# Performance work log

Measured on AMD Instinct MI355X. Metric: run time of the kernel, lower is better.

The kernel has to match this reference:

```python
import jax, jax.numpy as jnp
import numpy as np

N_NODES = 50000
N_EDGES = 800000
D = 64
L = 5
NUM_GRAPHS = 512
NOUT = 768

def setup_inputs() -> dict:
    key = jax.random.key(0)
    ks = jax.random.split(key, 8)
    s = 1.0 / np.sqrt(D)
    x = jax.random.normal(ks[0], (N_NODES, D), dtype=jnp.float32)
    edge_index = jax.random.randint(ks[1], (2, N_EDGES), 0, N_NODES, dtype=jnp.int64)
    batch = jnp.sort(jax.random.randint(ks[2], (N_NODES,), 0, NUM_GRAPHS, dtype=jnp.int64))
    return {
        'x': x,
        'edge_index': edge_index,
        'batch': batch,
        'gin_w1': jax.random.normal(ks[3], (L, D, D), dtype=jnp.float32) * s,
        'gin_b1': jnp.zeros((L, D), dtype=jnp.float32),
        'gin_w2': jax.random.normal(ks[4], (L, D, D), dtype=jnp.float32) * s,
        'gin_b2': jnp.zeros((L, D), dtype=jnp.float32),
        'eps': jnp.zeros((L,), dtype=jnp.float32),
        'w_h1': jax.random.normal(ks[5], (D, D), dtype=jnp.float32) * s,
        'b_h1': jnp.zeros((D,), dtype=jnp.float32),
        'w_h2': jax.random.normal(ks[6], (D, NOUT), dtype=jnp.float32) * s,
        'b_h2': jnp.zeros((NOUT,), dtype=jnp.float32),
    }

def reference(x, edge_index, batch, gin_w1, gin_b1, gin_w2, gin_b2, eps, w_h1, b_h1, w_h2, b_h2):
    src, dst = edge_index[0], edge_index[1]
    n = x.shape[0]
    h = x
    for l in range(L):
        # GINConv: mlp((1+eps)*x_i + sum_{j->i} x_j)  (scatter-add over edges)
        agg = jax.ops.segment_sum(h[src], dst, num_segments=n)
        z = (1.0 + eps[l]) * h + agg
        z = jax.nn.relu(z @ gin_w1[l] + gin_b1[l]) @ gin_w2[l] + gin_b2[l]
        h = jax.nn.relu(z) if l < L - 1 else z  # activation between conv layers only
    # global mean pool over graphs
    sums = jax.ops.segment_sum(h, batch, num_segments=NUM_GRAPHS)
    cnts = jax.ops.segment_sum(jnp.ones((n, 1), h.dtype), batch, num_segments=NUM_GRAPHS)
    pooled = sums / jnp.maximum(cnts, 1.0)
    # MLP head
    return jax.nn.relu(pooled @ w_h1 + b_h1) @ w_h2 + b_h2
```

## Files before the change

### kernel.cpp

```cpp
#include <hip/hip_runtime.h>
#include <hip/hip_fp16.h>

#define N_NODES 50000
#define N_EDGES 800000
#define D 64
#define NLAYER 5
#define NUM_GRAPHS 512
#define NOUT 768
#define ZSCALE 0.0625f
#define WSCALE 16.0f

#define SUPW 512
#define NSUPER 98
#define PART_EDGES 4096
#define PART_BLOCKS 196
#define CSR_CAP 16384

typedef _Float16 f16x8 __attribute__((ext_vector_type(8)));
typedef float f32x4 __attribute__((ext_vector_type(4)));


__global__ __launch_bounds__(128) void zero_super_kernel(int* __restrict__ superCnt) {
    int i = threadIdx.x;
    if (i < NSUPER) superCnt[i] = 0;
}

__global__ __launch_bounds__(256) void hist_super_kernel(const int* __restrict__ dst,
                                                         int* __restrict__ superCnt) {
    __shared__ int h[NSUPER];
    int t = threadIdx.x;
    if (t < NSUPER) h[t] = 0;
    __syncthreads();
    int e0 = blockIdx.x * PART_EDGES;
    int eN = min(e0 + PART_EDGES, N_EDGES) - e0;
    for (int i = t; i < eN; i += 256) atomicAdd(&h[dst[e0 + i] >> 9], 1);
    __syncthreads();
    if (t < NSUPER) atomicAdd(&superCnt[t], h[t]);
}

__global__ __launch_bounds__(128) void scan_super_kernel(const int* __restrict__ superCnt,
                                                         int* __restrict__ superBase,
                                                         int* __restrict__ superCur) {
    if (threadIdx.x == 0) {
        int run = 0;
        for (int s = 0; s < NSUPER; ++s) {
            superBase[s] = run; superCur[s] = run; run += superCnt[s];
        }
        superBase[NSUPER] = run;
    }
}

__global__ __launch_bounds__(1024) void partition_kernel(
    const int* __restrict__ src, const int* __restrict__ dst,
    int* __restrict__ superCur, unsigned* __restrict__ ebuf) {
    __shared__ int hist[NSUPER];
    __shared__ int pref[NSUPER + 1];
    __shared__ int base[NSUPER];
    __shared__ int curs[NSUPER];
    __shared__ unsigned out[PART_EDGES];
    int t = threadIdx.x;
    int e0 = blockIdx.x * PART_EDGES;
    int eN = min(e0 + PART_EDGES, N_EDGES) - e0;
    if (t < NSUPER) hist[t] = 0;
    __syncthreads();
    for (int i = t; i < eN; i += 1024) atomicAdd(&hist[dst[e0 + i] >> 9], 1);
    __syncthreads();
    if (t == 0) {
        int run = 0;
        for (int s = 0; s < NSUPER; ++s) { pref[s] = run; run += hist[s]; }
        pref[NSUPER] = run;
    }
    __syncthreads();
    if (t < NSUPER) {
        base[t] = atomicAdd(&superCur[t], hist[t]);
        curs[t] = pref[t];
    }
    __syncthreads();
    for (int i = t; i < eN; i += 1024) {
        int d = dst[e0 + i];
        int s = d >> 9;
        int p = atomicAdd(&curs[s], 1);
        out[p] = ((unsigned)(d & 511) << 16) | (unsigned)src[e0 + i];
    }
    __syncthreads();
    for (int i = t; i < eN; i += 1024) {
        int lo = 0, hi = NSUPER;
        while (lo + 1 < hi) { int mid = (lo + hi) >> 1; if (pref[mid] <= i) lo = mid; else hi = mid; }
        ebuf[base[lo] + (i - pref[lo])] = out[i];
    }
}

__global__ __launch_bounds__(512) void buildcsr_kernel(const unsigned* __restrict__ ebuf,
                                                       const int* __restrict__ superBase,
                                                       unsigned short* __restrict__ csr16,
                                                       int* __restrict__ row_ptr) {
    __shared__ int hist[SUPW];
    __shared__ int pref[SUPW];
    __shared__ int cur[SUPW];
    __shared__ unsigned short out16[CSR_CAP];
    int s = blockIdx.x, t = threadIdx.x;
    int beg = superBase[s], end = superBase[s + 1];
    int cnt = end - beg;
    hist[t] = 0;
    __syncthreads();
    for (int i = beg + t; i < end; i += 512)
        atomicAdd(&hist[(ebuf[i] >> 16) & 511], 1);
    __syncthreads();
    pref[t] = hist[t];
    __syncthreads();
    #pragma unroll
    for (int off = 1; off < 512; off <<= 1) {
        int u = (t >= off) ? pref[t - off] : 0;
        __syncthreads();
        pref[t] += u;
        __syncthreads();
    }
    int excl = pref[t] - hist[t];
    int node = s * SUPW + t;
    if (node < N_NODES) row_ptr[node] = beg + excl;
    if (s == NSUPER - 1 && t == 0) row_ptr[N_NODES] = N_EDGES;
    cur[t] = excl;
    __syncthreads();
    for (int i = beg + t; i < end; i += 512) {
        unsigned u = ebuf[i];
        int p = atomicAdd(&cur[(u >> 16) & 511], 1);
        unsigned short sv = (unsigned short)(u & 0xffff);
        if (p < CSR_CAP) out16[p] = sv;
        else csr16[beg + p] = sv;
    }
    __syncthreads();
    int lim = min(cnt, CSR_CAP);
    for (int i = t; i < lim; i += 512) csr16[beg + i] = out16[i];
}

__global__ __launch_bounds__(256) void tohalf_kernel(const float* __restrict__ in,
                                                     __half2* __restrict__ out) {
    int i = blockIdx.x * 256 + threadIdx.x;
    if (i < N_NODES * D / 2) {
        float2 v = ((const float2*)in)[i];
        out[i] = __floats2half2_rn(v.x, v.y);
    }
}

template <bool LAST>
__global__ __launch_bounds__(256, 4) void gin_fused_kernel(
    const __half2* __restrict__ h2in, __half2* __restrict__ h16out,
    float* __restrict__ hout_f32,
    const int* __restrict__ row_ptr, const unsigned short* __restrict__ csr16,
    const float* __restrict__ eps, int l,
    const float* __restrict__ w1, const float* __restrict__ b1,
    const float* __restrict__ w2, const float* __restrict__ b2) {
    __shared__ __align__(16) __half Z[D][72];
    __shared__ __align__(16) __half Wt[D][72];
    __shared__ float B1s[D], B2s[D];

    int t = threadIdx.x;
    int row0 = blockIdx.x * D;

    int nl = t >> 2;
    int q  = t & 3;
    int node = row0 + nl;
    bool nvalid = node < N_NODES;
    int beg = nvalid ? row_ptr[node] : 0;
    int end = nvalid ? row_ptr[node + 1] : 0;

    {
        const float4* ws = (const float4*)w1;
        #pragma unroll
        for (int i = 0; i < 4; ++i) {
            int g = t + i * 256;
            float4 v = ws[g];
            int k = g >> 4, n0 = (g & 15) << 2;
            Wt[n0 + 0][k] = __float2half_rn(v.x * WSCALE);
            Wt[n0 + 1][k] = __float2half_rn(v.y * WSCALE);
            Wt[n0 + 2][k] = __float2half_rn(v.z * WSCALE);
            Wt[n0 + 3][k] = __float2half_rn(v.w * WSCALE);
        }
        if (t < D) { B1s[t] = b1[t]; B2s[t] = b2[t]; }
    }

    float epsl = 1.0f + eps[l];
    const f16x8* hrows = (const f16x8*)h2in;

    float acc[16];
    {
        f16x8 u0 = {}, u1 = {};
        if (nvalid) {
            u0 = hrows[(size_t)node * 8 + 2 * q];
            u1 = hrows[(size_t)node * 8 + 2 * q + 1];
        }
        #pragma unroll
        for (int j = 0; j < 8; ++j) {
            acc[j]     = (float)u0[j] * epsl;
            acc[8 + j] = (float)u1[j] * epsl;
        }
    }
    for (int i = beg; i < end; i += 4) {
        #pragma unroll
        for (int k = 0; k < 4; ++k) {
            bool valid = (i + k < end);
            int ii = valid ? (i + k) : beg;
            float mult = valid ? 1.0f : 0.0f;
            int sidx = csr16[ii];
            f16x8 u0 = hrows[(size_t)sidx * 8 + 2 * q];
            f16x8 u1 = hrows[(size_t)sidx * 8 + 2 * q + 1];
            #pragma unroll
            for (int j = 0; j < 8; ++j) {
                acc[j]     = fmaf((float)u0[j], mult, acc[j]);
                acc[8 + j] = fmaf((float)u1[j], mult, acc[8 + j]);
            }
        }
    }
    {
        f16x8 z0, z1;
        #pragma unroll
        for (int j = 0; j < 8; ++j) {
            z0[j] = (_Float16)(acc[j] * ZSCALE);
            z1[j] = (_Float16)(acc[8 + j] * ZSCALE);
        }
        *(f16x8*)&Z[nl][q * 16]     = z0;
        *(f16x8*)&Z[nl][q * 16 + 8] = z1;
    }
    __syncthreads();

    int m  = t & 15;
    int hi = (t >> 4) & 3;
    int w  = t >> 6;

    float4 w2r[4];
    {
        const float4* ws = (const float4*)w2;
        #pragma unroll
        for (int i = 0; i < 4; ++i) w2r[i] = ws[t + i * 256];
    }

    f16x8 a0 = *(const f16x8*)&Z[w * 16 + m][hi * 8];
    f16x8 a1 = *(const f16x8*)&Z[w * 16 + m][32 + hi * 8];
    f32x4 c1[4];
    #pragma unroll
    for (int n = 0; n < 4; ++n) {
        f16x8 bf0 = *(const f16x8*)&Wt[n * 16 + m][hi * 8];
        f16x8 bf1 = *(const f16x8*)&Wt[n * 16 + m][32 + hi * 8];
        f32x4 c = {0.f, 0.f, 0.f, 0.f};
        c = __builtin_amdgcn_mfma_f32_16x16x32_f16(a0, bf0, c, 0, 0, 0);
        c = __builtin_amdgcn_mfma_f32_16x16x32_f16(a1, bf1, c, 0, 0, 0);
        c1[n] = c;
    }
    __syncthreads();

    #pragma unroll
    for (int n = 0; n < 4; ++n) {
        int col = n * 16 + m;
        #pragma unroll
        for (int r = 0; r < 4; ++r) {
            int row = w * 16 + hi * 4 + r;
            float v = c1[n][r] + B1s[col];
            Z[row][col] = __float2half_rn(fmaxf(v, 0.f) * ZSCALE);
        }
    }
    {
        #pragma unroll
        for (int i = 0; i < 4; ++i) {
            int g = t + i * 256;
            float4 v = w2r[i];
            int k = g >> 4, n0 = (g & 15) << 2;
            Wt[n0 + 0][k] = __float2half_rn(v.x * WSCALE);
            Wt[n0 + 1][k] = __float2half_rn(v.y * WSCALE);
            Wt[n0 + 2][k] = __float2half_rn(v.z * WSCALE);
            Wt[n0 + 3][k] = __float2half_rn(v.w * WSCALE);
        }
    }
    __syncthreads();

    f16x8 y0 = *(const f16x8*)&Z[w * 16 + m][hi * 8];
    f16x8 y1 = *(const f16x8*)&Z[w * 16 + m][32 + hi * 8];
    f32x4 c2[4];
    #pragma unroll
    for (int n = 0; n < 4; ++n) {
        f16x8 bf0 = *(const f16x8*)&Wt[n * 16 + m][hi * 8];
        f16x8 bf1 = *(const f16x8*)&Wt[n * 16 + m][32 + hi * 8];
        f32x4 c = {0.f, 0.f, 0.f, 0.f};
        c = __builtin_amdgcn_mfma_f32_16x16x32_f16(y0, bf0, c, 0, 0, 0);
        c = __builtin_amdgcn_mfma_f32_16x16x32_f16(y1, bf1, c, 0, 0, 0);
        c2[n] = c;
    }
    #pragma unroll
    for (int n = 0; n < 4; ++n) {
        int col = n * 16 + m;
        #pragma unroll
        for (int r = 0; r < 4; ++r) {
            int grow = row0 + w * 16 + hi * 4 + r;
            if (grow < N_NODES) {
                float o = c2[n][r] + B2s[col];
                if (LAST) {
                    hout_f32[(size_t)grow * D + col] = o;
                } else {
                    ((__half*)h16out)[(size_t)grow * D + col] = __float2half_rn(fmaxf(o, 0.f));
                }
            }
        }
    }
}

template <bool RELU>
__global__ __launch_bounds__(256) void gemm64_kernel(const float* __restrict__ X,
                                                     const float* __restrict__ Wg,
                                                     const float* __restrict__ bg,
                                                     float* __restrict__ Y, int nrows) {
    __shared__ float At[D][D + 1];
    __shared__ float Ws[D][D];
    __shared__ float Bs[D];

    int t = threadIdx.x;
    int row0 = blockIdx.x * D;
    {
        const float4* wsrc = (const float4*)Wg;
        float4* wdst = (float4*)Ws;
        #pragma unroll
        for (int i = 0; i < 4; ++i) wdst[t + i * 256] = wsrc[t + i * 256];
        if (t < D) Bs[t] = bg[t];
    }
    #pragma unroll
    for (int ii = 0; ii < 4; ++ii) {
        int i = t + ii * 256;
        int r = i >> 4;
        int c4 = i & 15;
        int row = row0 + r;
        float4 v = (row < nrows) ? ((const float4*)(X + (size_t)row * D))[c4]
                                 : make_float4(0.f, 0.f, 0.f, 0.f);
        At[c4 * 4 + 0][r] = v.x;
        At[c4 * 4 + 1][r] = v.y;
        At[c4 * 4 + 2][r] = v.z;
        At[c4 * 4 + 3][r] = v.w;
    }
    __syncthreads();

    int tx = t & 15, ty = t >> 4;
    int i0 = ty * 4, j0 = tx * 4;
    float acc[4][4];
    #pragma unroll
    for (int a = 0; a < 4; ++a)
        #pragma unroll
        for (int c = 0; c < 4; ++c) acc[a][c] = Bs[j0 + c];
    for (int k = 0; k < D; ++k) {
        float4 av = *(const float4*)&At[k][i0];
        float4 wv = *(const float4*)&Ws[k][j0];
        acc[0][0] += av.x * wv.x; acc[0][1] += av.x * wv.y; acc[0][2] += av.x * wv.z; acc[0][3] += av.x * wv.w;
        acc[1][0] += av.y * wv.x; acc[1][1] += av.y * wv.y; acc[1][2] += av.y * wv.z; acc[1][3] += av.y * wv.w;
        acc[2][0] += av.z * wv.x; acc[2][1] += av.z * wv.y; acc[2][2] += av.z * wv.z; acc[2][3] += av.z * wv.w;
        acc[3][0] += av.w * wv.x; acc[3][1] += av.w * wv.y; acc[3][2] += av.w * wv.z; acc[3][3] += av.w * wv.w;
    }
    #pragma unroll
    for (int a = 0; a < 4; ++a) {
        int row = row0 + i0 + a;
        if (row < nrows) {
            float4 v = make_float4(acc[a][0], acc[a][1], acc[a][2], acc[a][3]);
            if (RELU) {
                v.x = fmaxf(v.x, 0.f); v.y = fmaxf(v.y, 0.f);
                v.z = fmaxf(v.z, 0.f); v.w = fmaxf(v.w, 0.f);
            }
            ((float4*)(Y + (size_t)row * D))[tx] = v;
        }
    }
}

__device__ __forceinline__ int lower_bound_i(const int* a, int n, int key) {
    int lo = 0, hi = n;
    while (lo < hi) {
        int mid = (lo + hi) >> 1;
        if (a[mid] < key) lo = mid + 1;
        else hi = mid;
    }
    return lo;
}

__global__ __launch_bounds__(256) void pool_mean_kernel(const float* __restrict__ h,
                                                        const int* __restrict__ batch,
                                                        float* __restrict__ pooled) {
    __shared__ float red[4][D];
    int g = blockIdx.x;
    int t = threadIdx.x;
    int w = t >> 6, d = t & 63;
    int start = lower_bound_i(batch, N_NODES, g);
    int end = lower_bound_i(batch, N_NODES, g + 1);
    float sum = 0.f;
    for (int i = start + w; i < end; i += 4) sum += h[(size_t)i * D + d];
    red[w][d] = sum;
    __syncthreads();
    if (w == 0) {
        int cnt = end - start;
        float tot = red[0][d] + red[1][d] + red[2][d] + red[3][d];
        pooled[g * D + d] = tot / (float)(cnt > 0 ? cnt : 1);
    }
}

__global__ __launch_bounds__(256) void head2_kernel(const float* __restrict__ tin,
                                                    const float* __restrict__ w,
                                                    const float* __restrict__ b,
                                                    float* __restrict__ out) {
    __shared__ float trow[D];
    int i = blockIdx.y;
    int j = blockIdx.x * 256 + threadIdx.x;
    if (threadIdx.x < D) trow[threadIdx.x] = tin[i * D + threadIdx.x];
    __syncthreads();
    float acc = b[j];
    #pragma unroll
    for (int k = 0; k < D; ++k) acc += trow[k] * w[k * NOUT + j];
    out[(size_t)i * NOUT + j] = acc;
}

extern "C" void kernel_launch(void* const* d_in, const int* in_sizes, int n_in,
                              void* d_out, int out_size, void* d_ws, size_t ws_size,
                              hipStream_t stream) {
    const float* x   = (const float*)d_in[0];
    const int*   ei  = (const int*)d_in[1];
    const int*   src = ei;
    const int*   dst = ei + N_EDGES;
    const int* batch = (const int*)d_in[2];
    const float* gw1 = (const float*)d_in[3];
    const float* gb1 = (const float*)d_in[4];
    const float* gw2 = (const float*)d_in[5];
    const float* gb2 = (const float*)d_in[6];
    const float* eps = (const float*)d_in[7];
    const float* wh1 = (const float*)d_in[8];
    const float* bh1 = (const float*)d_in[9];
    const float* wh2 = (const float*)d_in[10];
    const float* bh2 = (const float*)d_in[11];
    float* out = (float*)d_out;

    char* p = (char*)d_ws;
    float* hfin   = (float*)p; p += (size_t)N_NODES * D * 4;
    float* pooled = (float*)p; p += (size_t)NUM_GRAPHS * D * 4;
    float* thead  = (float*)p; p += (size_t)NUM_GRAPHS * D * 4;
    __half2* h16a = (__half2*)p; p += (size_t)N_NODES * D * 2;
    __half2* h16b = (__half2*)p; p += (size_t)N_NODES * D * 2;
    unsigned* ebuf = (unsigned*)p; p += (size_t)N_EDGES * 4;
    int* superCnt  = (int*)p; p += 128 * 4;
    int* superBase = (int*)p; p += 128 * 4;
    int* superCur  = (int*)p; p += 128 * 4;
    int* row_ptr   = (int*)p; p += 50052 * 4;
    unsigned short* csr16 = (unsigned short*)p; p += (size_t)N_EDGES * 2;

    const int nodeBlocks = (N_NODES + D - 1) / D;

    zero_super_kernel<<<1, 128, 0, stream>>>(superCnt);
    hist_super_kernel<<<PART_BLOCKS, 256, 0, stream>>>(dst, superCnt);
    scan_super_kernel<<<1, 128, 0, stream>>>(superCnt, superBase, superCur);
    partition_kernel<<<PART_BLOCKS, 1024, 0, stream>>>(src, dst, superCur, ebuf);
    buildcsr_kernel<<<NSUPER, 512, 0, stream>>>(ebuf, superBase, csr16, row_ptr);

    tohalf_kernel<<<(N_NODES * D / 2 + 255) / 256, 256, 0, stream>>>(x, h16a);

    const __half2* hin = h16a;
    __half2* hout = h16b;
    for (int l = 0; l < NLAYER; ++l) {
        if (l < NLAYER - 1)
            gin_fused_kernel<false><<<nodeBlocks, 256, 0, stream>>>(
                hin, hout, hfin, row_ptr, csr16, eps, l,
                gw1 + (size_t)l * D * D, gb1 + (size_t)l * D,
                gw2 + (size_t)l * D * D, gb2 + (size_t)l * D);
        else
            gin_fused_kernel<true><<<nodeBlocks, 256, 0, stream>>>(
                hin, hout, hfin, row_ptr, csr16, eps, l,
                gw1 + (size_t)l * D * D, gb1 + (size_t)l * D,
                gw2 + (size_t)l * D * D, gb2 + (size_t)l * D);
        const __half2* tmp = hin;
        hin = hout;
        hout = (__half2*)tmp;
    }

    pool_mean_kernel<<<NUM_GRAPHS, 256, 0, stream>>>(hfin, batch, pooled);
    gemm64_kernel<true><<<(NUM_GRAPHS + D - 1) / D, 256, 0, stream>>>(pooled, wh1, bh1, thead, NUM_GRAPHS);
    head2_kernel<<<dim3(NOUT / 256, NUM_GRAPHS), 256, 0, stream>>>(thead, wh2, bh2, out);
}
```

Before: 167.9 us.

## Fuse tail kernels, shrink GIN tile, and streamline CSR build

The fp16 conversion of x moves into the histogram kernel, and each packed edge now carries its superbin so the binary search disappears. The block scan is replaced with wave shuffles. The GIN layer uses 32-node tiles with 8 threads per node and batches 8 gathered rows per iteration for more memory parallelism and occupancy. Pooling and both head GEMMs are fused into one 32-block kernel, which cuts launches but makes the tail much less parallel.

Result: slower. 330.6 us (+96.9%).

```diff
diff --git a/kernel.cpp b/kernel.cpp
--- a/kernel.cpp
+++ b/kernel.cpp
@@ -16,6 +16,9 @@
 #define PART_BLOCKS 196
 #define CSR_CAP 16384
 
+#define GIN_TILE 32
+#define GIN_BLOCKS 1563
+
 typedef _Float16 f16x8 __attribute__((ext_vector_type(8)));
 typedef float f32x4 __attribute__((ext_vector_type(4)));
 
@@ -26,11 +29,21 @@
 }
 
 __global__ __launch_bounds__(256) void hist_super_kernel(const int* __restrict__ dst,
-                                                         int* __restrict__ superCnt) {
+                                                         int* __restrict__ superCnt,
+                                                         const float* __restrict__ xin,
+                                                         __half2* __restrict__ xh) {
     __shared__ int h[NSUPER];
     int t = threadIdx.x;
     if (t < NSUPER) h[t] = 0;
     __syncthreads();
+    {
+        int gid = blockIdx.x * 256 + t;
+        int tot = N_NODES * D / 2;
+        for (int i = gid; i < tot; i += PART_BLOCKS * 256) {
+            float2 v = ((const float2*)xin)[i];
+            xh[i] = __floats2half2_rn(v.x, v.y);
+        }
+    }
     int e0 = blockIdx.x * PART_EDGES;
     int eN = min(e0 + PART_EDGES, N_EDGES) - e0;
     for (int i = t; i < eN; i += 256) atomicAdd(&h[dst[e0 + i] >> 9], 1);
@@ -80,13 +93,13 @@
         int d = dst[e0 + i];
         int s = d >> 9;
         int p = atomicAdd(&curs[s], 1);
-        out[p] = ((unsigned)(d & 511) << 16) | (unsigned)src[e0 + i];
+        out[p] = ((unsigned)s << 25) | ((unsigned)(d & 511) << 16) | (unsigned)src[e0 + i];
     }
     __syncthreads();
     for (int i = t; i < eN; i += 1024) {
-        int lo = 0, hi = NSUPER;
-        while (lo + 1 < hi) { int mid = (lo + hi) >> 1; if (pref[mid] <= i) lo = mid; else hi = mid; }
-        ebuf[base[lo] + (i - pref[lo])] = out[i];
+        unsigned u = out[i];
+        int s = u >> 25;
+        ebuf[base[s] + (i - pref[s])] = u;
     }
 }
 
@@ -95,10 +108,12 @@
                                                        unsigned short* __restrict__ csr16,
                                                        int* __restrict__ row_ptr) {
     __shared__ int hist[SUPW];
-    __shared__ int pref[SUPW];
     __shared__ int cur[SUPW];
+    __shared__ int waveSum[8];
+    __shared__ int waveOff[8];
     __shared__ unsigned short out16[CSR_CAP];
     int s = blockIdx.x, t = threadIdx.x;
+    int lane = t & 63, wv = t >> 6;
     int beg = superBase[s], end = superBase[s + 1];
     int cnt = end - beg;
     hist[t] = 0;
@@ -106,16 +121,22 @@
     for (int i = beg + t; i < end; i += 512)
         atomicAdd(&hist[(ebuf[i] >> 16) & 511], 1);
     __syncthreads();
-    pref[t] = hist[t];
-    __syncthreads();
+    int own = hist[t];
+    int x = own;
     #pragma unroll
-    for (int off = 1; off < 512; off <<= 1) {
-        int u = (t >= off) ? pref[t - off] : 0;
-        __syncthreads();
-        pref[t] += u;
-        __syncthreads();
-    }
-    int excl = pref[t] - hist[t];
+    for (int off = 1; off < 64; off <<= 1) {
+        int y = __shfl_up(x, off, 64);
+        if (lane >= off) x += y;
+    }
+    if (lane == 63) waveSum[wv] = x;
+    __syncthreads();
+    if (t == 0) {
+        int run = 0;
+        #pragma unroll
+        for (int w = 0; w < 8; ++w) { waveOff[w] = run; run += waveSum[w]; }
+    }
+    __syncthreads();
+    int excl = x + waveOff[wv] - own;
     int node = s * SUPW + t;
     if (node < N_NODES) row_ptr[node] = beg + excl;
     if (s == NSUPER - 1 && t == 0) row_ptr[N_NODES] = N_EDGES;
@@ -133,32 +154,23 @@
     for (int i = t; i < lim; i += 512) csr16[beg + i] = out16[i];
 }
 
-__global__ __launch_bounds__(256) void tohalf_kernel(const float* __restrict__ in,
-                                                     __half2* __restrict__ out) {
-    int i = blockIdx.x * 256 + threadIdx.x;
-    if (i < N_NODES * D / 2) {
-        float2 v = ((const float2*)in)[i];
-        out[i] = __floats2half2_rn(v.x, v.y);
-    }
-}
-
 template <bool LAST>
-__global__ __launch_bounds__(256, 4) void gin_fused_kernel(
+__global__ __launch_bounds__(256, 6) void gin_fused_kernel(
     const __half2* __restrict__ h2in, __half2* __restrict__ h16out,
     float* __restrict__ hout_f32,
     const int* __restrict__ row_ptr, const unsigned short* __restrict__ csr16,
     const float* __restrict__ eps, int l,
     const float* __restrict__ w1, const float* __restrict__ b1,
     const float* __restrict__ w2, const float* __restrict__ b2) {
-    __shared__ __align__(16) __half Z[D][72];
+    __shared__ __align__(16) __half Z[GIN_TILE][72];
     __shared__ __align__(16) __half Wt[D][72];
     __shared__ float B1s[D], B2s[D];
 
     int t = threadIdx.x;
-    int row0 = blockIdx.x * D;
-
-    int nl = t >> 2;
-    int q  = t & 3;
+    int row0 = blockIdx.x * GIN_TILE;
+
+    int nl = t >> 3;
+    int o  = t & 7;
     int node = row0 + nl;
     bool nvalid = node < N_NODES;
     int beg = nvalid ? row_ptr[node] : 0;
@@ -182,50 +194,45 @@
     float epsl = 1.0f + eps[l];
     const f16x8* hrows = (const f16x8*)h2in;
 
-    float acc[16];
-    {
-        f16x8 u0 = {}, u1 = {};
-        if (nvalid) {
-            u0 = hrows[(size_t)node * 8 + 2 * q];
-            u1 = hrows[(size_t)node * 8 + 2 * q + 1];
-        }
-        #pragma unroll
-        for (int j = 0; j < 8; ++j) {
-            acc[j]     = (float)u0[j] * epsl;
-            acc[8 + j] = (float)u1[j] * epsl;
-        }
-    }
-    for (int i = beg; i < end; i += 4) {
-        #pragma unroll
-        for (int k = 0; k < 4; ++k) {
+    float acc[8];
+    {
+        f16x8 u = {};
+        if (nvalid) u = hrows[(size_t)node * 8 + o];
+        #pragma unroll
+        for (int j = 0; j < 8; ++j) acc[j] = (float)u[j] * epsl;
+    }
+    for (int i = beg; i < end; i += 8) {
+        int sidx[8]; float mult[8];
+        #pragma unroll
+        for (int k = 0; k < 8; ++k) {
             bool valid = (i + k < end);
             int ii = valid ? (i + k) : beg;
-            float mult = valid ? 1.0f : 0.0f;
-            int sidx = csr16[ii];
-            f16x8 u0 = hrows[(size_t)sidx * 8 + 2 * q];
-            f16x8 u1 = hrows[(size_t)sidx * 8 + 2 * q + 1];
+            mult[k] = valid ? 1.0f : 0.0f;
+            sidx[k] = csr16[ii];
+        }
+        f16x8 u[8];
+        #pragma unroll
+        for (int k = 0; k < 8; ++k) u[k] = hrows[(size_t)sidx[k] * 8 + o];
+        #pragma unroll
+        for (int k = 0; k < 8; ++k)
             #pragma unroll
-            for (int j = 0; j < 8; ++j) {
-                acc[j]     = fmaf((float)u0[j], mult, acc[j]);
-                acc[8 + j] = fmaf((float)u1[j], mult, acc[8 + j]);
-            }
-        }
-    }
-    {
-        f16x8 z0, z1;
-        #pragma unroll
-        for (int j = 0; j < 8; ++j) {
-            z0[j] = (_Float16)(acc[j] * ZSCALE);
-            z1[j] = (_Float16)(acc[8 + j] * ZSCALE);
-        }
-        *(f16x8*)&Z[nl][q * 16]     = z0;
-        *(f16x8*)&Z[nl][q * 16 + 8] = z1;
-    }
-    __syncthreads();
-
-    int m  = t & 15;
-    int hi = (t >> 4) & 3;
-    int w  = t >> 6;
+            for (int j = 0; j < 8; ++j)
+                acc[j] = fmaf((float)u[k][j], mult[k], acc[j]);
+    }
+    {
+        f16x8 z;
+        #pragma unroll
+        for (int j = 0; j < 8; ++j) z[j] = (_Float16)(acc[j] * ZSCALE);
+        *(f16x8*)&Z[nl][o * 8] = z;
+    }
+    __syncthreads();
+
+    int lane = t & 63;
+    int v  = t >> 6;
+    int m  = lane & 15;
+    int hi = lane >> 4;
+    int mt = v & 1;
+    int np = v >> 1;
 
     float4 w2r[4];
     {
@@ -234,132 +241,72 @@
         for (int i = 0; i < 4; ++i) w2r[i] = ws[t + i * 256];
     }
 
-    f16x8 a0 = *(const f16x8*)&Z[w * 16 + m][hi * 8];
-    f16x8 a1 = *(const f16x8*)&Z[w * 16 + m][32 + hi * 8];
-    f32x4 c1[4];
+    f16x8 a0 = *(const f16x8*)&Z[mt * 16 + m][hi * 8];
+    f16x8 a1 = *(const f16x8*)&Z[mt * 16 + m][32 + hi * 8];
+    f32x4 c1[2];
     #pragma unroll
-    for (int n = 0; n < 4; ++n) {
+    for (int nn = 0; nn < 2; ++nn) {
+        int n = np * 2 + nn;
         f16x8 bf0 = *(const f16x8*)&Wt[n * 16 + m][hi * 8];
         f16x8 bf1 = *(const f16x8*)&Wt[n * 16 + m][32 + hi * 8];
         f32x4 c = {0.f, 0.f, 0.f, 0.f};
         c = __builtin_amdgcn_mfma_f32_16x16x32_f16(a0, bf0, c, 0, 0, 0);
         c = __builtin_amdgcn_mfma_f32_16x16x32_f16(a1, bf1, c, 0, 0, 0);
-        c1[n] = c;
+        c1[nn] = c;
     }
     __syncthreads();
 
     #pragma unroll
-    for (int n = 0; n < 4; ++n) {
-        int col = n * 16 + m;
+    for (int nn = 0; nn < 2; ++nn) {
+        int col = (np * 2 + nn) * 16 + m;
         #pragma unroll
         for (int r = 0; r < 4; ++r) {
-            int row = w * 16 + hi * 4 + r;
-            float v = c1[n][r] + B1s[col];
-            Z[row][col] = __float2half_rn(fmaxf(v, 0.f) * ZSCALE);
+            int row = mt * 16 + hi * 4 + r;
+            float val = c1[nn][r] + B1s[col];
+            Z[row][col] = __float2half_rn(fmaxf(val, 0.f) * ZSCALE);
         }
     }
     {
         #pragma unroll
         for (int i = 0; i < 4; ++i) {
             int g = t + i * 256;
-            float4 v = w2r[i];
+            float4 vv = w2r[i];
             int k = g >> 4, n0 = (g & 15) << 2;
-            Wt[n0 + 0][k] = __float2half_rn(v.x * WSCALE);
-            Wt[n0 + 1][k] = __float2half_rn(v.y * WSCALE);
-            Wt[n0 + 2][k] = __float2half_rn(v.z * WSCALE);
-            Wt[n0 + 3][k] = __float2half_rn(v.w * WSCALE);
-        }
-    }
-    __syncthreads();
-
-    f16x8 y0 = *(const f16x8*)&Z[w * 16 + m][hi * 8];
-    f16x8 y1 = *(const f16x8*)&Z[w * 16 + m][32 + hi * 8];
-    f32x4 c2[4];
+            Wt[n0 + 0][k] = __float2half_rn(vv.x * WSCALE);
+            Wt[n0 + 1][k] = __float2half_rn(vv.y * WSCALE);
+            Wt[n0 + 2][k] = __float2half_rn(vv.z * WSCALE);
+            Wt[n0 + 3][k] = __float2half_rn(vv.w * WSCALE);
+        }
+    }
+    __syncthreads();
+
+    f16x8 y0 = *(const f16x8*)&Z[mt * 16 + m][hi * 8];
+    f16x8 y1 = *(const f16x8*)&Z[mt * 16 + m][32 + hi * 8];
+    f32x4 c2[2];
     #pragma unroll
-    for (int n = 0; n < 4; ++n) {
+    for (int nn = 0; nn < 2; ++nn) {
+        int n = np * 2 + nn;
         f16x8 bf0 = *(const f16x8*)&Wt[n * 16 + m][hi * 8];
         f16x8 bf1 = *(const f16x8*)&Wt[n * 16 + m][32 + hi * 8];
         f32x4 c = {0.f, 0.f, 0.f, 0.f};
         c = __builtin_amdgcn_mfma_f32_16x16x32_f16(y0, bf0, c, 0, 0, 0);
         c = __builtin_amdgcn_mfma_f32_16x16x32_f16(y1, bf1, c, 0, 0, 0);
-        c2[n] = c;
+        c2[nn] = c;
     }
     #pragma unroll
-    for (int n = 0; n < 4; ++n) {
-        int col = n * 16 + m;
+    for (int nn = 0; nn < 2; ++nn) {
+        int col = (np * 2 + nn) * 16 + m;
         #pragma unroll
         for (int r = 0; r < 4; ++r) {
-            int grow = row0 + w * 16 + hi * 4 + r;
+            int grow = row0 + mt * 16 + hi * 4 + r;
             if (grow < N_NODES) {
-                float o = c2[n][r] + B2s[col];
+                float ov = c2[nn][r] + B2s[col];
                 if (LAST) {
-                    hout_f32[(size_t)grow * D + col] = o;
+                    hout_f32[(size_t)grow * D + col] = ov;
                 } else {
-                    ((__half*)h16out)[(size_t)grow * D + col] = __float2half_rn(fmaxf(o, 0.f));
+                    ((__half*)h16out)[(size_t)grow * D + col] = __float2half_rn(fmaxf(ov, 0.f));
                 }
             }
-        }
-    }
-}
-
-template <bool RELU>
-__global__ __launch_bounds__(256) void gemm64_kernel(const float* __restrict__ X,
-                                                     const float* __restrict__ Wg,
-                                                     const float* __restrict__ bg,
-                                                     float* __restrict__ Y, int nrows) {
-    __shared__ float At[D][D + 1];
-    __shared__ float Ws[D][D];
-    __shared__ float Bs[D];
-
-    int t = threadIdx.x;
-    int row0 = blockIdx.x * D;
-    {
-        const float4* wsrc = (const float4*)Wg;
-        float4* wdst = (float4*)Ws;
-        #pragma unroll
-        for (int i = 0; i < 4; ++i) wdst[t + i * 256] = wsrc[t + i * 256];
-        if (t < D) Bs[t] = bg[t];
-    }
-    #pragma unroll
-    for (int ii = 0; ii < 4; ++ii) {
-        int i = t + ii * 256;
-        int r = i >> 4;
-        int c4 = i & 15;
-        int row = row0 + r;
-        float4 v = (row < nrows) ? ((const float4*)(X + (size_t)row * D))[c4]
-                                 : make_float4(0.f, 0.f, 0.f, 0.f);
-        At[c4 * 4 + 0][r] = v.x;
-        At[c4 * 4 + 1][r] = v.y;
-        At[c4 * 4 + 2][r] = v.z;
-        At[c4 * 4 + 3][r] = v.w;
-    }
-    __syncthreads();
-
-    int tx = t & 15, ty = t >> 4;
-    int i0 = ty * 4, j0 = tx * 4;
-    float acc[4][4];
-    #pragma unroll
-    for (int a = 0; a < 4; ++a)
-        #pragma unroll
-        for (int c = 0; c < 4; ++c) acc[a][c] = Bs[j0 + c];
-    for (int k = 0; k < D; ++k) {
-        float4 av = *(const float4*)&At[k][i0];
-        float4 wv = *(const float4*)&Ws[k][j0];
-        acc[0][0] += av.x * wv.x; acc[0][1] += av.x * wv.y; acc[0][2] += av.x * wv.z; acc[0][3] += av.x * wv.w;
-        acc[1][0] += av.y * wv.x; acc[1][1] += av.y * wv.y; acc[1][2] += av.y * wv.z; acc[1][3] += av.y * wv.w;
-        acc[2][0] += av.z * wv.x; acc[2][1] += av.z * wv.y; acc[2][2] += av.z * wv.z; acc[2][3] += av.z * wv.w;
-        acc[3][0] += av.w * wv.x; acc[3][1] += av.w * wv.y; acc[3][2] += av.w * wv.z; acc[3][3] += av.w * wv.w;
-    }
-    #pragma unroll
-    for (int a = 0; a < 4; ++a) {
-        int row = row0 + i0 + a;
-        if (row < nrows) {
-            float4 v = make_float4(acc[a][0], acc[a][1], acc[a][2], acc[a][3]);
-            if (RELU) {
-                v.x = fmaxf(v.x, 0.f); v.y = fmaxf(v.y, 0.f);
-                v.z = fmaxf(v.z, 0.f); v.w = fmaxf(v.w, 0.f);
-            }
-            ((float4*)(Y + (size_t)row * D))[tx] = v;
         }
     }
 }
@@ -374,39 +321,69 @@
     return lo;
 }
 
-__global__ __launch_bounds__(256) void pool_mean_kernel(const float* __restrict__ h,
-                                                        const int* __restrict__ batch,
-                                                        float* __restrict__ pooled) {
-    __shared__ float red[4][D];
-    int g = blockIdx.x;
+#define TAIL_G 16
+__global__ __launch_bounds__(256) void pool_head_kernel(
+    const float* __restrict__ hfin, const int* __restrict__ batch,
+    const float* __restrict__ wh1, const float* __restrict__ bh1,
+    const float* __restrict__ wh2, const float* __restrict__ bh2,
+    float* __restrict__ out) {
+    __shared__ float P[TAIL_G][D + 1];
+    __shared__ float Wh[D * D];
+    __shared__ float T[TAIL_G][D + 1];
+
     int t = threadIdx.x;
+    int g0 = blockIdx.x * TAIL_G;
     int w = t >> 6, d = t & 63;
-    int start = lower_bound_i(batch, N_NODES, g);
-    int end = lower_bound_i(batch, N_NODES, g + 1);
-    float sum = 0.f;
-    for (int i = start + w; i < end; i += 4) sum += h[(size_t)i * D + d];
-    red[w][d] = sum;
-    __syncthreads();
-    if (w == 0) {
-        int cnt = end - start;
-        float tot = red[0][d] + red[1][d] + red[2][d] + red[3][d];
-        pooled[g * D + d] = tot / (float)(cnt > 0 ? cnt : 1);
-    }
-}
-
-__global__ __launch_bounds__(256) void head2_kernel(const float* __restrict__ tin,
-                                                    const float* __restrict__ w,
-                                                    const float* __restrict__ b,
-                                                    float* __restrict__ out) {
-    __shared__ float trow[D];
-    int i = blockIdx.y;
-    int j = blockIdx.x * 256 + threadIdx.x;
-    if (threadIdx.x < D) trow[threadIdx.x] = tin[i * D + threadIdx.x];
-    __syncthreads();
-    float acc = b[j];
-    #pragma unroll
-    for (int k = 0; k < D; ++k) acc += trow[k] * w[k * NOUT + j];
-    out[(size_t)i * NOUT + j] = acc;
+
+    {
+        const float4* ws = (const float4*)wh1;
+        float4* wd = (float4*)Wh;
+        #pragma unroll
+        for (int i = 0; i < 4; ++i) wd[t + i * 256] = ws[t + i * 256];
+    }
+
+    for (int gi = w; gi < TAIL_G; gi += 4) {
+        int g = g0 + gi;
+        int start = lower_bound_i(batch, N_NODES, g);
+        int fin   = lower_bound_i(batch, N_NODES, g + 1);
+        float s = 0.f;
+        for (int i = start; i < fin; ++i) s += hfin[(size_t)i * D + d];
+        int cnt = fin - start;
+        P[gi][d] = s / (float)(cnt > 0 ? cnt : 1);
+    }
+    __syncthreads();
+
+    {
+        int r0 = w * 4;
+        float a0 = bh1[d], a1 = a0, a2 = a0, a3 = a0;
+        for (int k = 0; k < D; ++k) {
+            float wv = Wh[k * D + d];
+            a0 = fmaf(P[r0 + 0][k], wv, a0);
+            a1 = fmaf(P[r0 + 1][k], wv, a1);
+            a2 = fmaf(P[r0 + 2][k], wv, a2);
+            a3 = fmaf(P[r0 + 3][k], wv, a3);
+        }
+        T[r0 + 0][d] = fmaxf(a0, 0.f);
+        T[r0 + 1][d] = fmaxf(a1, 0.f);
+        T[r0 + 2][d] = fmaxf(a2, 0.f);
+        T[r0 + 3][d] = fmaxf(a3, 0.f);
+    }
+    __syncthreads();
+
+    for (int cg = 0; cg < NOUT / 256; ++cg) {
+        int j = cg * 256 + t;
+        float wcol[D];
+        #pragma unroll
+        for (int k = 0; k < D; ++k) wcol[k] = wh2[(size_t)k * NOUT + j];
+        float bj = bh2[j];
+        #pragma unroll 4
+        for (int r = 0; r < TAIL_G; ++r) {
+            float a = bj;
+            #pragma unroll
+            for (int k = 0; k < D; ++k) a = fmaf(T[r][k], wcol[k], a);
+            out[(size_t)(g0 + r) * NOUT + j] = a;
+        }
+    }
 }
 
 extern "C" void kernel_launch(void* const* d_in, const int* in_sizes, int n_in,
@@ -440,27 +417,24 @@
     int* superCur  = (int*)p; p += 128 * 4;
     int* row_ptr   = (int*)p; p += 50052 * 4;
     unsigned short* csr16 = (unsigned short*)p; p += (size_t)N_EDGES * 2;
-
-    const int nodeBlocks = (N_NODES + D - 1) / D;
+    (void)pooled; (void)thead;
 
     zero_super_kernel<<<1, 128, 0, stream>>>(superCnt);
-    hist_super_kernel<<<PART_BLOCKS, 256, 0, stream>>>(dst, superCnt);
+    hist_super_kernel<<<PART_BLOCKS, 256, 0, stream>>>(dst, superCnt, x, h16a);
     scan_super_kernel<<<1, 128, 0, stream>>>(superCnt, superBase, superCur);
     partition_kernel<<<PART_BLOCKS, 1024, 0, stream>>>(src, dst, superCur, ebuf);
     buildcsr_kernel<<<NSUPER, 512, 0, stream>>>(ebuf, superBase, csr16, row_ptr);
-
-    tohalf_kernel<<<(N_NODES * D / 2 + 255) / 256, 256, 0, stream>>>(x, h16a);
 
     const __half2* hin = h16a;
     __half2* hout = h16b;
     for (int l = 0; l < NLAYER; ++l) {
         if (l < NLAYER - 1)
-            gin_fused_kernel<false><<<nodeBlocks, 256, 0, stream>>>(
+            gin_fused_kernel<false><<<GIN_BLOCKS, 256, 0, stream>>>(
                 hin, hout, hfin, row_ptr, csr16, eps, l,
                 gw1 + (size_t)l * D * D, gb1 + (size_t)l * D,
                 gw2 + (size_t)l * D * D, gb2 + (size_t)l * D);
         else
-            gin_fused_kernel<true><<<nodeBlocks, 256, 0, stream>>>(
+            gin_fused_kernel<true><<<GIN_BLOCKS, 256, 0, stream>>>(
                 hin, hout, hfin, row_ptr, csr16, eps, l,
                 gw1 + (size_t)l * D * D, gb1 + (size_t)l * D,
                 gw2 + (size_t)l * D * D, gb2 + (size_t)l * D);
@@ -469,7 +443,6 @@
         hout = (__half2*)tmp;
     }
 
-    pool_mean_kernel<<<NUM_GRAPHS, 256, 0, stream>>>(hfin, batch, pooled);
-    gemm64_kernel<true><<<(NUM_GRAPHS + D - 1) / D, 256, 0, stream>>>(pooled, wh1, bh1, thead, NUM_GRAPHS);
-    head2_kernel<<<dim3(NOUT / 256, NUM_GRAPHS), 256, 0, stream>>>(thead, wh2, bh2, out);
-}
+    pool_head_kernel<<<NUM_GRAPHS / TAIL_G, 256, 0, stream>>>(
+        hfin, batch, wh1, bh1, wh2, bh2, out);
+}
```
